# Kernel tuning notes

Measured on AMD Instinct MI355X. Metric: run time of the kernel, lower is better.

Reference implementation:

```python
import jax, jax.numpy as jnp
import numpy as np

NUM_HEADS = 4
LN_EPS = 1e-5


def _gcn_layer(src, dst, feats, skip_w, skip_b, msg_w, msg_b):
    # DGL GCNLayer: symmetric degree norm (from src rows), copy_u+sum aggregation,
    # msg linear + affine skip. No activation is applied in the original forward.
    n = feats.shape[0]
    deg = jax.ops.segment_sum(jnp.ones(src.shape, feats.dtype), src, num_segments=n)
    dinv = jnp.where(deg > 0, deg ** -0.5, jnp.zeros_like(deg))
    h = feats * dinv[:, None]                                  # [N, D]
    agg = jax.ops.segment_sum(h[src], dst, num_segments=n)     # scatter-sum over edges
    rst = agg * dinv[:, None]
    return rst @ msg_w.T + msg_b + feats @ skip_w.T + skip_b


def _layernorm(x, g, b):
    mu = jnp.mean(x, axis=-1, keepdims=True)
    var = jnp.mean((x - mu) ** 2, axis=-1, keepdims=True)
    return (x - mu) * jax.lax.rsqrt(var + LN_EPS) * g + b


def _cross_attention(x, seq, in_proj_w, in_proj_b, out_proj_w, out_proj_b, ln_g, ln_b):
    # Unbatched torch nn.MultiheadAttention(query=x [N,D], key=value=seq [S,D]).
    n, d = x.shape
    hd = d // NUM_HEADS
    wq, wk, wv = in_proj_w[:d], in_proj_w[d:2 * d], in_proj_w[2 * d:]
    bq, bk, bv = in_proj_b[:d], in_proj_b[d:2 * d], in_proj_b[2 * d:]
    q = (x @ wq.T + bq).reshape(n, NUM_HEADS, hd)
    k = (seq @ wk.T + bk).reshape(-1, NUM_HEADS, hd)
    v = (seq @ wv.T + bv).reshape(-1, NUM_HEADS, hd)
    scores = jnp.einsum('nhd,shd->hns', q, k) / jnp.sqrt(jnp.asarray(hd, x.dtype))
    attn = jax.nn.softmax(scores, axis=-1)
    o = jnp.einsum('hns,shd->nhd', attn, v).reshape(n, d)
    o = o @ out_proj_w.T + out_proj_b
    # dropout is identity in eval mode; residual + layernorm (num_cross_att == 1 path)
    return _layernorm(o + x, ln_g, ln_b)


def reference(x, seq_embeddings, src, dst, edge_label_index,
              skip_w0, skip_b0, msg_w0, msg_b0,
              skip_w1, skip_b1, msg_w1, msg_b1,
              in_proj_w, in_proj_b, out_proj_w, out_proj_b, ln_g, ln_b,
              weight1, weight2):
    x = _gcn_layer(src, dst, x, skip_w0, skip_b0, msg_w0, msg_b0)
    x = _gcn_layer(src, dst, x, skip_w1, skip_b1, msg_w1, msg_b1)
    x = _cross_attention(x, seq_embeddings, in_proj_w, in_proj_b,
                         out_proj_w, out_proj_b, ln_g, ln_b)
    # F.normalize: row-wise L2
    x = x / jnp.maximum(jnp.linalg.norm(x, axis=-1, keepdims=True), 1e-12)
    node_embedding = x
    p = jax.nn.relu(x @ weight1.T)                # dropout identity (eval)
    p = jax.nn.sigmoid(p @ weight2.T)[:, 0]       # [N]
    # dot edge decoding over last dim of size 1 -> elementwise product
    pred = p[edge_label_index[0]] * p[edge_label_index[1]]
    return pred, node_embedding


def setup_inputs() -> dict:
    key = jax.random.key(0)
    ks = jax.random.split(key, 20)
    N, E, S, D, K = 8192, 524288, 2048, 128, 100000
    s = 1.0 / np.sqrt(D)  # xavier-ish scale for weight matrices
    inp = {
        'x': jax.random.normal(ks[0], (N, D), jnp.float32),
        'seq_embeddings': jax.random.normal(ks[1], (S, D), jnp.float32),
        'src': jax.random.randint(ks[2], (E,), 0, N, jnp.int32),
        'dst': jax.random.randint(ks[3], (E,), 0, N, jnp.int32),
        'edge_label_index': jax.random.randint(ks[4], (2, K), 0, N, jnp.int32),
        'skip_w0': jax.random.normal(ks[5], (D, D), jnp.float32) * s,
        'skip_b0': jnp.zeros((D,), jnp.float32),
        'msg_w0': jax.random.normal(ks[6], (D, D), jnp.float32) * s,
        'msg_b0': jnp.zeros((D,), jnp.float32),
        'skip_w1': jax.random.normal(ks[7], (D, D), jnp.float32) * s,
        'skip_b1': jnp.zeros((D,), jnp.float32),
        'msg_w1': jax.random.normal(ks[8], (D, D), jnp.float32) * s,
        'msg_b1': jnp.zeros((D,), jnp.float32),
        'in_proj_w': jax.random.normal(ks[9], (3 * D, D), jnp.float32) * s,
        'in_proj_b': jnp.zeros((3 * D,), jnp.float32),
        'out_proj_w': jax.random.normal(ks[10], (D, D), jnp.float32) * s,
        'out_proj_b': jnp.zeros((D,), jnp.float32),
        'ln_g': jnp.ones((D,), jnp.float32),
        'ln_b': jnp.zeros((D,), jnp.float32),
        'weight1': jax.random.normal(ks[11], (D, D), jnp.float32) * s,
        'weight2': jax.random.normal(ks[12], (1, D), jnp.float32) * s,
    }
    return inp
```

## Files before the change

kernel.cpp:

```cpp
#include <hip/hip_runtime.h>
#include <math.h>

#define D 128
#define HB 128
#define FA_PS 88
#define SPLITS 4

typedef short bf16x4 __attribute__((ext_vector_type(4)));
typedef short bf16x8 __attribute__((ext_vector_type(8)));
typedef float f32x4 __attribute__((ext_vector_type(4)));

__device__ __forceinline__ float4 ld4(const float* p) { return *(const float4*)p; }

__device__ __forceinline__ short f2bf_r(float f) {
  return (short)((__float_as_uint(f) + 0x8000u) >> 16);
}
__device__ __forceinline__ float bf2f(short s) {
  return __uint_as_float(((unsigned)(unsigned short)s) << 16);
}
__device__ __forceinline__ unsigned pack_bf2(float a, float b) {
  unsigned ua = __float_as_uint(a) + 0x8000u;
  unsigned ub = __float_as_uint(b) + 0x8000u;
  return __builtin_amdgcn_perm(ub, ua, 0x07060302);
}

struct WSrc { const float* p[9]; };
__global__ __launch_bounds__(256) void prep_hist_kernel(
    WSrc ws, short* __restrict__ Wbf,
    const float* __restrict__ x, short* __restrict__ xbf, int* __restrict__ MkhI,
    const int* __restrict__ src, const int* __restrict__ dst,
    int* __restrict__ histd, int* __restrict__ hists, int E, int NB_COPY) {
  __shared__ int hd[8192];
  __shared__ int hs[8192];
  int b = blockIdx.x, t = threadIdx.x;
  if (b < NB_COPY) {
    if (b == 0 && t < 4) MkhI[t] = 0;
    if (b < 144) {
      int m = b >> 4, blk = b & 15;
      int i = (blk * 256 + t) * 4;
      float4 v = ld4(ws.p[m] + i);
      bf16x4 o = {f2bf_r(v.x), f2bf_r(v.y), f2bf_r(v.z), f2bf_r(v.w)};
      *(bf16x4*)&Wbf[m * 16384 + i] = o;
    } else {
      int i = ((b - 144) * 256 + t) * 4;
      float4 v = ld4(x + i);
      bf16x4 o = {f2bf_r(v.x), f2bf_r(v.y), f2bf_r(v.z), f2bf_r(v.w)};
      *(bf16x4*)&xbf[i] = o;
    }
    return;
  }
  int hb = b - NB_COPY;
  for (int i = t; i < 8192; i += 256) { hd[i] = 0; hs[i] = 0; }
  __syncthreads();
  int per = E / HB;
  int b0 = hb * per;
  for (int j = 0; j < per; j += 256) {
    int i = b0 + j + t;
    atomicAdd(&hd[dst[i]], 1);
    atomicAdd(&hs[src[i]], 1);
  }
  __syncthreads();
  for (int i = t; i < 8192; i += 256) {
    histd[hb * 8192 + i] = hd[i];
    hists[hb * 8192 + i] = hs[i];
  }
}

__global__ __launch_bounds__(256) void colsum_kernel(
    const int* __restrict__ histd, const int* __restrict__ hists,
    int* __restrict__ deg, float* __restrict__ dinv) {
  int v = blockIdx.x * 256 + threadIdx.x;
  int sd = 0, ss = 0;
  for (int b = 0; b < HB; ++b) { sd += histd[b * 8192 + v]; ss += hists[b * 8192 + v]; }
  deg[v] = sd;
  dinv[v] = ss > 0 ? rsqrtf((float)ss) : 0.f;
}

__global__ __launch_bounds__(1024) void scan8k_kernel(
    const int* __restrict__ deg, int* __restrict__ row_ptr, int N) {
  __shared__ int wtot[16];
  int t = threadIdx.x;
  int lane = t & 63, wv = t >> 6;
  int v0 = t * 8;
  int x[8]; int s = 0;
#pragma unroll
  for (int j = 0; j < 8; ++j) { x[j] = s; s += deg[v0 + j]; }
  int incl = s;
  for (int off = 1; off < 64; off <<= 1) {
    int y = __shfl_up(incl, off);
    if (lane >= off) incl += y;
  }
  if (lane == 63) wtot[wv] = incl;
  __syncthreads();
  if (t == 0) { int run = 0; for (int i = 0; i < 16; ++i) { int v = wtot[i]; wtot[i] = run; run += v; } }
  __syncthreads();
  int base = wtot[wv] + (incl - s);
#pragma unroll
  for (int j = 0; j < 8; ++j) row_ptr[v0 + j] = base + x[j];
  if (t == 1023) row_ptr[N] = base + s;
}

__global__ __launch_bounds__(256) void basegen_kernel(
    const int* __restrict__ histd, const int* __restrict__ row_ptr,
    int* __restrict__ base_arr) {
  int v = blockIdx.x * 256 + threadIdx.x;
  int run = row_ptr[v];
  for (int b = 0; b < HB; ++b) { base_arr[b * 8192 + v] = run; run += histd[b * 8192 + v]; }
}

__global__ __launch_bounds__(256) void scatter2_kernel(
    const int* __restrict__ src, const int* __restrict__ dst,
    const int* __restrict__ base_arr, int* __restrict__ csr_src, int E) {
  __shared__ int lh[8192];
  int t = threadIdx.x;
  for (int i = t; i < 8192; i += 256) lh[i] = 0;
  __syncthreads();
  int per = E / HB;
  int b0 = blockIdx.x * per;
  const int* __restrict__ bb = &base_arr[blockIdx.x * 8192];
  for (int j = 0; j < per; j += 256) {
    int i = b0 + j + t;
    int v = dst[i];
    int r = atomicAdd(&lh[v], 1);
    csr_src[bb[v] + r] = src[i];
  }
}

__global__ __launch_bounds__(128) void agg_kernel(
    const short* __restrict__ fbf, const float* __restrict__ dinv,
    const int* __restrict__ row_ptr, const int* __restrict__ csr_src,
    short* __restrict__ outbf) {
  __shared__ int idx[128];
  __shared__ float dv[128];
  __shared__ float red[8][128];
  int n = blockIdx.x, t = threadIdx.x;
  int grp = t >> 4, l16 = t & 15;
  int beg = row_ptr[n], end = row_ptr[n + 1];
  float a0[8] = {}, a1[8] = {}, a2[8] = {}, a3[8] = {};
  for (int c = beg; c < end; c += 128) {
    int j = c + t;
    if (j < end) { int s = csr_src[j]; idx[t] = s; dv[t] = dinv[s]; }
    __syncthreads();
    int cnt = min(128, end - c);
    int e = grp;
    for (; e + 24 < cnt; e += 32) {
      bf16x8 w0 = *(const bf16x8*)&fbf[(size_t)idx[e] * D + l16 * 8];
      bf16x8 w1 = *(const bf16x8*)&fbf[(size_t)idx[e + 8] * D + l16 * 8];
      bf16x8 w2 = *(const bf16x8*)&fbf[(size_t)idx[e + 16] * D + l16 * 8];
      bf16x8 w3 = *(const bf16x8*)&fbf[(size_t)idx[e + 24] * D + l16 * 8];
      float wt0 = dv[e], wt1 = dv[e + 8], wt2 = dv[e + 16], wt3 = dv[e + 24];
#pragma unroll
      for (int k = 0; k < 8; ++k) {
        a0[k] += bf2f(w0[k]) * wt0;
        a1[k] += bf2f(w1[k]) * wt1;
        a2[k] += bf2f(w2[k]) * wt2;
        a3[k] += bf2f(w3[k]) * wt3;
      }
    }
    for (; e < cnt; e += 8) {
      bf16x8 w0 = *(const bf16x8*)&fbf[(size_t)idx[e] * D + l16 * 8];
      float wt0 = dv[e];
#pragma unroll
      for (int k = 0; k < 8; ++k) a0[k] += bf2f(w0[k]) * wt0;
    }
    __syncthreads();
  }
#pragma unroll
  for (int k = 0; k < 8; ++k) a0[k] += a1[k] + a2[k] + a3[k];
  *(float4*)&red[grp][l16 * 8] = *(float4*)&a0[0];
  *(float4*)&red[grp][l16 * 8 + 4] = *(float4*)&a0[4];
  __syncthreads();
  if (t < 32) {
    int d0 = t * 4;
    float o[4] = {};
#pragma unroll
    for (int g = 0; g < 8; ++g) {
      o[0] += red[g][d0]; o[1] += red[g][d0 + 1];
      o[2] += red[g][d0 + 2]; o[3] += red[g][d0 + 3];
    }
    float w = dinv[n];
    bf16x4 ov = {f2bf_r(o[0] * w), f2bf_r(o[1] * w), f2bf_r(o[2] * w), f2bf_r(o[3] * w)};
    *(bf16x4*)&outbf[(size_t)n * D + d0] = ov;
  }
}

__device__ __forceinline__ void mfma_accum(const short* As, const short* __restrict__ W,
                                           int rt, int ch, int quad, int r16, f32x4* acc) {
#pragma unroll
  for (int ks = 0; ks < 4; ++ks) {
    bf16x8 af = *(bf16x8*)&As[(rt * 16 + r16) * 136 + ks * 32 + quad * 8];
#pragma unroll
    for (int nt = 0; nt < 4; ++nt) {
      bf16x8 bw = *(const bf16x8*)&W[(size_t)(ch * 64 + nt * 16 + r16) * D + ks * 32 + quad * 8];
      acc[nt] = __builtin_amdgcn_mfma_f32_16x16x32_bf16(af, bw, acc[nt], 0, 0, 0);
    }
  }
}

__device__ __forceinline__ void stage_A_f32(const float* __restrict__ A, int m0, short* As) {
  int row = threadIdx.x >> 3, seg = threadIdx.x & 7;
  const float* ap = &A[(size_t)(m0 + row) * D + seg * 16];
  float4 v0 = ld4(ap), v1 = ld4(ap + 4), v2 = ld4(ap + 8), v3 = ld4(ap + 12);
  bf16x8 w0 = {f2bf_r(v0.x), f2bf_r(v0.y), f2bf_r(v0.z), f2bf_r(v0.w),
               f2bf_r(v1.x), f2bf_r(v1.y), f2bf_r(v1.z), f2bf_r(v1.w)};
  bf16x8 w1 = {f2bf_r(v2.x), f2bf_r(v2.y), f2bf_r(v2.z), f2bf_r(v2.w),
               f2bf_r(v3.x), f2bf_r(v3.y), f2bf_r(v3.z), f2bf_r(v3.w)};
  *(bf16x8*)&As[row * 136 + seg * 16] = w0;
  *(bf16x8*)&As[row * 136 + seg * 16 + 8] = w1;
}

__device__ __forceinline__ void stage_A_bf16(const short* __restrict__ A, int m0, short* As) {
  int row = threadIdx.x >> 3, seg = threadIdx.x & 7;
  const short* ap = &A[(size_t)(m0 + row) * D + seg * 16];
  bf16x8 a0 = *(const bf16x8*)ap;
  bf16x8 a1 = *(const bf16x8*)(ap + 8);
  *(bf16x8*)&As[row * 136 + seg * 16] = a0;
  *(bf16x8*)&As[row * 136 + seg * 16 + 8] = a1;
}

__global__ __launch_bounds__(256) void gemm_gcn_kernel(
    const short* __restrict__ A1, const short* __restrict__ W1, const float* __restrict__ b1,
    const short* __restrict__ A2, const short* __restrict__ W2, const float* __restrict__ b2,
    short* __restrict__ Cbf, float* __restrict__ Cf) {
  __shared__ short As[32 * 136];
  const int t = threadIdx.x;
  const int m0 = blockIdx.x * 32;
  const int w = t >> 6, lane = t & 63, quad = lane >> 4, r16 = lane & 15;
  const int rt = w & 1, ch = w >> 1;
  f32x4 acc[4];
  f32x4 zz = {0.f, 0.f, 0.f, 0.f};
  acc[0] = zz; acc[1] = zz; acc[2] = zz; acc[3] = zz;
  stage_A_bf16(A1, m0, As);
  __syncthreads();
  mfma_accum(As, W1, rt, ch, quad, r16, acc);
  __syncthreads();
  stage_A_bf16(A2, m0, As);
  __syncthreads();
  mfma_accum(As, W2, rt, ch, quad, r16, acc);
#pragma unroll
  for (int nt = 0; nt < 4; ++nt) {
    int col = ch * 64 + nt * 16 + r16;
    float bias = b1[col] + b2[col];
#pragma unroll
    for (int g = 0; g < 4; ++g) {
      int row = m0 + rt * 16 + quad * 4 + g;
      float v = acc[nt][g] + bias;
      if (Cbf) Cbf[(size_t)row * D + col] = f2bf_r(v);
      if (Cf) Cf[(size_t)row * D + col] = v;
    }
  }
}

__global__ __launch_bounds__(256) void qkv_kernel(
    const float* __restrict__ B2, const float* __restrict__ seq,
    const short* __restrict__ Wq, const short* __restrict__ Wk, const short* __restrict__ Wv,
    const float* __restrict__ ipb,
    short* __restrict__ Qh, float* __restrict__ qn,
    short* __restrict__ Kh, int* __restrict__ MkhI,
    short* __restrict__ Vt, int N, int S) {
  __shared__ short As[32 * 136];
  __shared__ int lmax[4];
  const int t = threadIdx.x;
  const int b = blockIdx.x;
  const int w = t >> 6, lane = t & 63, quad = lane >> 4, r16 = lane & 15;
  const int rt = w & 1, ch = w >> 1;
  if (t < 4) lmax[t] = 0;
  f32x4 acc[4];
  f32x4 zz = {0.f, 0.f, 0.f, 0.f};
  acc[0] = zz; acc[1] = zz; acc[2] = zz; acc[3] = zz;
  const float SC = 0.25503473f;

  if (b < 256) {
    int m0 = b * 32;
    stage_A_f32(B2, m0, As);
    __syncthreads();
    mfma_accum(As, Wq, rt, ch, quad, r16, acc);
    float pq[4][2] = {};
#pragma unroll
    for (int nt = 0; nt < 4; ++nt) {
      int col = ch * 64 + nt * 16 + r16;
      int hq = col >> 5, dq = col & 31;
      float bias = ipb[col];
      int p = nt >> 1;
#pragma unroll
      for (int g = 0; g < 4; ++g) {
        int row = m0 + rt * 16 + quad * 4 + g;
        float vs = (acc[nt][g] + bias) * SC;
        Qh[((size_t)hq * N + row) * 32 + dq] = f2bf_r(vs);
        pq[g][p] += vs * vs;
      }
    }
#pragma unroll
    for (int mask = 1; mask < 16; mask <<= 1)
#pragma unroll
      for (int g = 0; g < 4; ++g) {
        pq[g][0] += __shfl_xor(pq[g][0], mask);
        pq[g][1] += __shfl_xor(pq[g][1], mask);
      }
    if (r16 == 0) {
#pragma unroll
      for (int g = 0; g < 4; ++g) {
        int row = m0 + rt * 16 + quad * 4 + g;
        qn[(ch * 2 + 0) * N + row] = sqrtf(pq[g][0]);
        qn[(ch * 2 + 1) * N + row] = sqrtf(pq[g][1]);
      }
    }
  } else if (b < 320) {
    int m0 = (b - 256) * 32;
    stage_A_f32(seq, m0, As);
    __syncthreads();
    mfma_accum(As, Wk, rt, ch, quad, r16, acc);
    float pk[4][2] = {};
#pragma unroll
    for (int nt = 0; nt < 4; ++nt) {
      int col = ch * 64 + nt * 16 + r16;
      int hk = col >> 5, dk = col & 31;
      float bias = ipb[128 + col];
      int p = nt >> 1;
#pragma unroll
      for (int g = 0; g < 4; ++g) {
        int key = m0 + rt * 16 + quad * 4 + g;
        float v = acc[nt][g] + bias;
        Kh[((size_t)hk * S + key) * 32 + dk] = f2bf_r(v);
        pk[g][p] += v * v;
      }
    }
#pragma unroll
    for (int mask = 1; mask < 16; mask <<= 1)
#pragma unroll
      for (int g = 0; g < 4; ++g) {
        pk[g][0] += __shfl_xor(pk[g][0], mask);
        pk[g][1] += __shfl_xor(pk[g][1], mask);
      }
    if (r16 == 0) {
#pragma unroll
      for (int g = 0; g < 4; ++g) {
        atomicMax(&lmax[ch * 2 + 0], __float_as_int(pk[g][0]));
        atomicMax(&lmax[ch * 2 + 1], __float_as_int(pk[g][1]));
      }
    }
    __syncthreads();
    if (t < 4) atomicMax(&MkhI[t], lmax[t]);
  } else {
    int m0 = (b - 320) * 32;
    stage_A_f32(seq, m0, As);
    __syncthreads();
    mfma_accum(As, Wv, rt, ch, quad, r16, acc);
#pragma unroll
    for (int nt = 0; nt < 4; ++nt) {
      int dim = ch * 64 + nt * 16 + r16;
      float bias = ipb[256 + dim];
#pragma unroll
      for (int g = 0; g < 4; ++g) {
        int s = m0 + rt * 16 + quad * 4 + g;
        int local = s & 63;
        int kp = (local & 15) * 4 + (local >> 4);
        int gcol = (s & ~63) + kp;
        Vt[(size_t)dim * S + gcol] = f2bf_r(acc[nt][g] + bias);
      }
    }
  }
}

__global__ __launch_bounds__(128, 8) void flash_kernel(
    const short* __restrict__ Qh, const short* __restrict__ Kh, const short* __restrict__ Vt,
    const float* __restrict__ qn, const int* __restrict__ MkhI,
    float* __restrict__ Osp, float* __restrict__ lbuf, int N, int S) {
  __shared__ short Ps[2][32 * FA_PS];
  const int wv = threadIdx.x >> 6;
  const int lane = threadIdx.x & 63;
  const int quad = lane >> 4, r16 = lane & 15;
  const int n0 = (blockIdx.x * 2 + wv) * 32;
  const int h = blockIdx.y;
  const int sp = blockIdx.z;
  float* O = Osp + (size_t)sp * N * D;
  const short* Kb = Kh + (size_t)h * S * 32;
  const short* Qb = Qh + (size_t)h * N * 32;
  short* Pw = Ps[wv];

  bf16x8 aq[2];
  aq[0] = *(const bf16x8*)&Qb[(size_t)(n0 + r16) * 32 + quad * 8];
  aq[1] = *(const bf16x8*)&Qb[(size_t)(n0 + 16 + r16) * 32 + quad * 8];

  float sqm = sqrtf(fmaxf(__int_as_float(MkhI[h]), 0.f));
  float msh[2][4];
#pragma unroll
  for (int rt = 0; rt < 2; ++rt)
#pragma unroll
    for (int g = 0; g < 4; ++g)
      msh[rt][g] = fminf(qn[h * N + n0 + rt * 16 + quad * 4 + g] * sqm, 57.7f);

  f32x4 o[2][2], lac[2];
  f32x4 zz = {0.f, 0.f, 0.f, 0.f};
  o[0][0] = zz; o[0][1] = zz; o[1][0] = zz; o[1][1] = zz;
  lac[0] = zz; lac[1] = zz;
  bf16x8 ones = {(short)0x3F80, (short)0x3F80, (short)0x3F80, (short)0x3F80,
                 (short)0x3F80, (short)0x3F80, (short)0x3F80, (short)0x3F80};

  const int span = S / SPLITS;
  const int c0 = sp * span;
  for (int c = c0; c < c0 + span; c += 64) {
    f32x4 s[2][4];
#pragma unroll
    for (int kt = 0; kt < 4; ++kt) {
      bf16x8 bk = *(const bf16x8*)&Kb[(size_t)(c + kt * 16 + r16) * 32 + quad * 8];
      f32x4 z = {0.f, 0.f, 0.f, 0.f};
      s[0][kt] = __builtin_amdgcn_mfma_f32_16x16x32_bf16(aq[0], bk, z, 0, 0, 0);
      s[1][kt] = __builtin_amdgcn_mfma_f32_16x16x32_bf16(aq[1], bk, z, 0, 0, 0);
    }
#pragma unroll
    for (int rt = 0; rt < 2; ++rt)
#pragma unroll
      for (int g = 0; g < 4; ++g) {
        float m = msh[rt][g];
        float p0 = exp2f(s[rt][0][g] - m);
        float p1 = exp2f(s[rt][1][g] - m);
        float p2 = exp2f(s[rt][2][g] - m);
        float p3 = exp2f(s[rt][3][g] - m);
        uint2 uv = {pack_bf2(p0, p1), pack_bf2(p2, p3)};
        *(uint2*)&Pw[(rt * 16 + quad * 4 + g) * FA_PS + r16 * 4] = uv;
      }
    bf16x8 bv[2][2];
#pragma unroll
    for (int kc = 0; kc < 2; ++kc)
#pragma unroll
      for (int nt = 0; nt < 2; ++nt)
        bv[kc][nt] = *(const bf16x8*)&Vt[(size_t)(h * 32 + nt * 16 + r16) * S + c + kc * 32 + quad * 8];
#pragma unroll
    for (int rt = 0; rt < 2; ++rt)
#pragma unroll
      for (int kc = 0; kc < 2; ++kc) {
        bf16x8 ap = *(bf16x8*)&Pw[(rt * 16 + r16) * FA_PS + kc * 32 + quad * 8];
        lac[rt] = __builtin_amdgcn_mfma_f32_16x16x32_bf16(ap, ones, lac[rt], 0, 0, 0);
#pragma unroll
        for (int nt = 0; nt < 2; ++nt)
          o[rt][nt] = __builtin_amdgcn_mfma_f32_16x16x32_bf16(ap, bv[kc][nt], o[rt][nt], 0, 0, 0);
      }
  }
#pragma unroll
  for (int rt = 0; rt < 2; ++rt)
#pragma unroll
    for (int g = 0; g < 4; ++g) {
      int row = n0 + rt * 16 + quad * 4 + g;
#pragma unroll
      for (int nt = 0; nt < 2; ++nt)
        O[(size_t)row * D + h * 32 + nt * 16 + r16] = o[rt][nt][g];
      if (r16 == 0) lbuf[(sp * 4 + h) * N + row] = lac[rt][g];
    }
}

__global__ __launch_bounds__(256) void gemm_op_kernel(
    const float* __restrict__ Osp, const float* __restrict__ lbuf,
    const short* __restrict__ W, const float* __restrict__ bias,
    const float* __restrict__ Rres, const float* __restrict__ ln_g,
    const float* __restrict__ ln_b, float* __restrict__ emb, int N) {
  __shared__ short As[32 * 136];
  __shared__ float Cs[32 * 132];
  const int t = threadIdx.x;
  const int m0 = blockIdx.x * 32;
  const int w = t >> 6, lane = t & 63, quad = lane >> 4, r16 = lane & 15;
  const int rt = w & 1, ch = w >> 1;
  {
    int row = t >> 3, seg = t & 7;
    int grow = m0 + row;
    int hh = seg >> 1;
    float l = 0.f;
#pragma unroll
    for (int s = 0; s < SPLITS; ++s) l += lbuf[(s * 4 + hh) * N + grow];
    float inv = 1.f / l;
    const float* p = &Osp[(size_t)grow * D + seg * 16];
    size_t st = (size_t)N * D;
    float a16[16] = {};
#pragma unroll
    for (int s = 0; s < SPLITS; ++s) {
#pragma unroll
      for (int q = 0; q < 4; ++q) {
        float4 a = ld4(p + s * st + q * 4);
        a16[q * 4 + 0] += a.x; a16[q * 4 + 1] += a.y;
        a16[q * 4 + 2] += a.z; a16[q * 4 + 3] += a.w;
      }
    }
#pragma unroll
    for (int k = 0; k < 16; ++k) a16[k] *= inv;
    bf16x8 w0 = {f2bf_r(a16[0]), f2bf_r(a16[1]), f2bf_r(a16[2]), f2bf_r(a16[3]),
                 f2bf_r(a16[4]), f2bf_r(a16[5]), f2bf_r(a16[6]), f2bf_r(a16[7])};
    bf16x8 w1 = {f2bf_r(a16[8]), f2bf_r(a16[9]), f2bf_r(a16[10]), f2bf_r(a16[11]),
                 f2bf_r(a16[12]), f2bf_r(a16[13]), f2bf_r(a16[14]), f2bf_r(a16[15])};
    *(bf16x8*)&As[row * 136 + seg * 16] = w0;
    *(bf16x8*)&As[row * 136 + seg * 16 + 8] = w1;
  }
  __syncthreads();
  f32x4 acc[4];
  f32x4 zz = {0.f, 0.f, 0.f, 0.f};
  acc[0] = zz; acc[1] = zz; acc[2] = zz; acc[3] = zz;
  mfma_accum(As, W, rt, ch, quad, r16, acc);
#pragma unroll
  for (int nt = 0; nt < 4; ++nt) {
    int col = ch * 64 + nt * 16 + r16;
    float bs = bias[col];
#pragma unroll
    for (int g = 0; g < 4; ++g) {
      int lr = rt * 16 + quad * 4 + g;
      Cs[lr * 132 + col] = acc[nt][g] + bs + Rres[(size_t)(m0 + lr) * D + col];
    }
  }
  __syncthreads();
  {
    int row = t >> 3, seg = t & 7;
    float xv[16];
#pragma unroll
    for (int q = 0; q < 4; ++q) {
      f32x4 v = *(f32x4*)&Cs[row * 132 + seg * 16 + q * 4];
      xv[q * 4] = v[0]; xv[q * 4 + 1] = v[1]; xv[q * 4 + 2] = v[2]; xv[q * 4 + 3] = v[3];
    }
    float s = 0.f, sq = 0.f;
#pragma unroll
    for (int k = 0; k < 16; ++k) { s += xv[k]; sq += xv[k] * xv[k]; }
#pragma unroll
    for (int mask = 1; mask < 8; mask <<= 1) { s += __shfl_xor(s, mask); sq += __shfl_xor(sq, mask); }
    float mu = s * (1.f / 128.f);
    float var = fmaxf(sq * (1.f / 128.f) - mu * mu, 0.f);
    float rs = rsqrtf(var + 1e-5f);
    float yv[16], nn = 0.f;
#pragma unroll
    for (int q = 0; q < 4; ++q) {
      float4 gg = ld4(&ln_g[seg * 16 + q * 4]);
      float4 bb = ld4(&ln_b[seg * 16 + q * 4]);
      float y0 = (xv[q * 4] - mu) * rs * gg.x + bb.x;
      float y1 = (xv[q * 4 + 1] - mu) * rs * gg.y + bb.y;
      float y2 = (xv[q * 4 + 2] - mu) * rs * gg.z + bb.z;
      float y3 = (xv[q * 4 + 3] - mu) * rs * gg.w + bb.w;
      yv[q * 4] = y0; yv[q * 4 + 1] = y1; yv[q * 4 + 2] = y2; yv[q * 4 + 3] = y3;
      nn += y0 * y0 + y1 * y1 + y2 * y2 + y3 * y3;
    }
#pragma unroll
    for (int mask = 1; mask < 8; mask <<= 1) nn += __shfl_xor(nn, mask);
    float inv = 1.f / fmaxf(sqrtf(nn), 1e-12f);
#pragma unroll
    for (int q = 0; q < 4; ++q) {
      float4 ov = {yv[q * 4] * inv, yv[q * 4 + 1] * inv, yv[q * 4 + 2] * inv, yv[q * 4 + 3] * inv};
      *(float4*)&emb[(size_t)(m0 + row) * D + seg * 16 + q * 4] = ov;
    }
  }
}

__global__ __launch_bounds__(256) void gemm_mlp_kernel(
    const float* __restrict__ emb, const short* __restrict__ W,
    const float* __restrict__ w2, float* __restrict__ pbuf) {
  __shared__ short As[32 * 136];
  __shared__ float part[32][2];
  const int t = threadIdx.x;
  const int m0 = blockIdx.x * 32;
  const int w = t >> 6, lane = t & 63, quad = lane >> 4, r16 = lane & 15;
  const int rt = w & 1, ch = w >> 1;
  stage_A_f32(emb, m0, As);
  __syncthreads();
  f32x4 acc[4];
  f32x4 zz = {0.f, 0.f, 0.f, 0.f};
  acc[0] = zz; acc[1] = zz; acc[2] = zz; acc[3] = zz;
  mfma_accum(As, W, rt, ch, quad, r16, acc);
  float pg[4] = {};
#pragma unroll
  for (int nt = 0; nt < 4; ++nt) {
    float wv = w2[ch * 64 + nt * 16 + r16];
#pragma unroll
    for (int g = 0; g < 4; ++g) pg[g] += fmaxf(acc[nt][g], 0.f) * wv;
  }
#pragma unroll
  for (int mask = 1; mask < 16; mask <<= 1)
#pragma unroll
    for (int g = 0; g < 4; ++g) pg[g] += __shfl_xor(pg[g], mask);
  if (r16 == 0) {
#pragma unroll
    for (int g = 0; g < 4; ++g) part[rt * 16 + quad * 4 + g][ch] = pg[g];
  }
  __syncthreads();
  if (t < 32) {
    float sv = part[t][0] + part[t][1];
    pbuf[m0 + t] = 1.f / (1.f + __expf(-sv));
  }
}

__global__ void pred_kernel(const float* __restrict__ p, const int* __restrict__ eli,
                            float* __restrict__ out, int K) {
  int i = blockIdx.x * blockDim.x + threadIdx.x;
  if (i < K) out[i] = p[eli[i]] * p[eli[K + i]];
}

extern "C" void kernel_launch(void* const* d_in, const int* in_sizes, int n_in,
                              void* d_out, int out_size, void* d_ws, size_t ws_size,
                              hipStream_t stream) {
  const float* x       = (const float*)d_in[0];
  const float* seq     = (const float*)d_in[1];
  const int* src       = (const int*)d_in[2];
  const int* dst       = (const int*)d_in[3];
  const int* eli       = (const int*)d_in[4];
  const float* skip_w0 = (const float*)d_in[5];
  const float* skip_b0 = (const float*)d_in[6];
  const float* msg_w0  = (const float*)d_in[7];
  const float* msg_b0  = (const float*)d_in[8];
  const float* skip_w1 = (const float*)d_in[9];
  const float* skip_b1 = (const float*)d_in[10];
  const float* msg_w1  = (const float*)d_in[11];
  const float* msg_b1  = (const float*)d_in[12];
  const float* ipw     = (const float*)d_in[13];
  const float* ipb     = (const float*)d_in[14];
  const float* opw     = (const float*)d_in[15];
  const float* opb     = (const float*)d_in[16];
  const float* ln_g    = (const float*)d_in[17];
  const float* ln_b    = (const float*)d_in[18];
  const float* w1      = (const float*)d_in[19];
  const float* w2      = (const float*)d_in[20];

  const int N  = in_sizes[0] / D;
  const int S  = in_sizes[1] / D;
  const int E  = in_sizes[2];
  const int Kp = in_sizes[4] / 2;

  float* ws    = (float*)d_ws;
  float* B2    = ws;
  float* Osp   = B2 + (size_t)N * D;
  short* xbf   = (short*)(Osp + (size_t)SPLITS * N * D);
  short* Abf   = xbf + (size_t)N * D;
  short* B1bf  = Abf + (size_t)N * D;
  short* Qh    = B1bf + (size_t)N * D;
  short* Kh    = Qh + (size_t)N * D;
  short* Vt    = Kh + (size_t)S * D;
  short* Wbf   = Vt + (size_t)D * S;
  float* qn    = (float*)(Wbf + 9 * 16384);
  float* lbuf  = qn + 4 * (size_t)N;
  float* dinv  = lbuf + 4 * (size_t)SPLITS * N;
  float* pbuf  = dinv + N;
  int*   MkhI  = (int*)(pbuf + N);
  int*   deg   = MkhI + 4;
  int* row_ptr = deg + N;
  int* csr_src = row_ptr + (N + 1);
  int* histd   = csr_src + E;
  int* hists   = histd + HB * 8192;
  int* base_arr= hists + HB * 8192;

  float* pred_out = (float*)d_out;
  float* emb_out  = pred_out + Kp;

  const short* w_skip0 = Wbf + 0 * 16384;
  const short* w_msg0  = Wbf + 1 * 16384;
  const short* w_skip1 = Wbf + 2 * 16384;
  const short* w_msg1  = Wbf + 3 * 16384;
  const short* w_q     = Wbf + 4 * 16384;
  const short* w_k     = Wbf + 5 * 16384;
  const short* w_v     = Wbf + 6 * 16384;
  const short* w_op    = Wbf + 7 * 16384;
  const short* w_m1    = Wbf + 8 * 16384;

  WSrc wsrc;
  wsrc.p[0] = skip_w0; wsrc.p[1] = msg_w0; wsrc.p[2] = skip_w1; wsrc.p[3] = msg_w1;
  wsrc.p[4] = ipw; wsrc.p[5] = ipw + D * D; wsrc.p[6] = ipw + 2 * D * D;
  wsrc.p[7] = opw; wsrc.p[8] = w1;

  const int NB_COPY = 144 + (N * D / 1024);
  prep_hist_kernel<<<NB_COPY + HB, 256, 0, stream>>>(
      wsrc, (short*)Wbf, x, xbf, MkhI, src, dst, histd, hists, E, NB_COPY);

  colsum_kernel<<<N / 256, 256, 0, stream>>>(histd, hists, deg, dinv);
  scan8k_kernel<<<1, 1024, 0, stream>>>(deg, row_ptr, N);
  basegen_kernel<<<N / 256, 256, 0, stream>>>(histd, row_ptr, base_arr);
  scatter2_kernel<<<HB, 256, 0, stream>>>(src, dst, base_arr, csr_src, E);

  agg_kernel<<<N, 128, 0, stream>>>(xbf, dinv, row_ptr, csr_src, Abf);
  gemm_gcn_kernel<<<N / 32, 256, 0, stream>>>(Abf, w_msg0, msg_b0, xbf, w_skip0, skip_b0, B1bf, nullptr);
  agg_kernel<<<N, 128, 0, stream>>>(B1bf, dinv, row_ptr, csr_src, Abf);
  gemm_gcn_kernel<<<N / 32, 256, 0, stream>>>(Abf, w_msg1, msg_b1, B1bf, w_skip1, skip_b1, nullptr, B2);

  qkv_kernel<<<N / 32 + 2 * (S / 32), 256, 0, stream>>>(
      B2, seq, w_q, w_k, w_v, ipb, Qh, qn, Kh, MkhI, Vt, N, S);

  dim3 fgrid(N / 64, 4, SPLITS);
  flash_kernel<<<fgrid, 128, 0, stream>>>(Qh, Kh, Vt, qn, MkhI, Osp, lbuf, N, S);
  gemm_op_kernel<<<N / 32, 256, 0, stream>>>(Osp, lbuf, w_op, opb, B2, ln_g, ln_b, emb_out, N);

  gemm_mlp_kernel<<<N / 32, 256, 0, stream>>>(emb_out, w_m1, w2, pbuf);
  pred_kernel<<<(Kp + 255) / 256, 256, 0, stream>>>(pbuf, eli, pred_out, Kp);
}
```

Baseline: 238.7 us.

## Fuse Q projection into GCN GEMM, fuse MLP into out-proj, shrink histograms

```diff
diff --git a/kernel.cpp b/kernel.cpp
--- a/kernel.cpp
+++ b/kernel.cpp
@@ -29,7 +29,8 @@
     WSrc ws, short* __restrict__ Wbf,
     const float* __restrict__ x, short* __restrict__ xbf, int* __restrict__ MkhI,
     const int* __restrict__ src, const int* __restrict__ dst,
-    int* __restrict__ histd, int* __restrict__ hists, int E, int NB_COPY) {
+    unsigned short* __restrict__ histd, unsigned short* __restrict__ hists,
+    int E, int NB_COPY) {
   __shared__ int hd[8192];
   __shared__ int hs[8192];
   int b = blockIdx.x, t = threadIdx.x;
@@ -61,13 +62,13 @@
   }
   __syncthreads();
   for (int i = t; i < 8192; i += 256) {
-    histd[hb * 8192 + i] = hd[i];
-    hists[hb * 8192 + i] = hs[i];
+    histd[hb * 8192 + i] = (unsigned short)hd[i];
+    hists[hb * 8192 + i] = (unsigned short)hs[i];
   }
 }
 
 __global__ __launch_bounds__(256) void colsum_kernel(
-    const int* __restrict__ histd, const int* __restrict__ hists,
+    const unsigned short* __restrict__ histd, const unsigned short* __restrict__ hists,
     int* __restrict__ deg, float* __restrict__ dinv) {
   int v = blockIdx.x * 256 + threadIdx.x;
   int sd = 0, ss = 0;
@@ -101,7 +102,7 @@
 }
 
 __global__ __launch_bounds__(256) void basegen_kernel(
-    const int* __restrict__ histd, const int* __restrict__ row_ptr,
+    const unsigned short* __restrict__ histd, const int* __restrict__ row_ptr,
     int* __restrict__ base_arr) {
   int v = blockIdx.x * 256 + threadIdx.x;
   int run = row_ptr[v];
@@ -221,7 +222,7 @@
 __global__ __launch_bounds__(256) void gemm_gcn_kernel(
     const short* __restrict__ A1, const short* __restrict__ W1, const float* __restrict__ b1,
     const short* __restrict__ A2, const short* __restrict__ W2, const float* __restrict__ b2,
-    short* __restrict__ Cbf, float* __restrict__ Cf) {
+    short* __restrict__ Cbf) {
   __shared__ short As[32 * 136];
   const int t = threadIdx.x;
   const int m0 = blockIdx.x * 32;
@@ -244,20 +245,87 @@
 #pragma unroll
     for (int g = 0; g < 4; ++g) {
       int row = m0 + rt * 16 + quad * 4 + g;
+      Cbf[(size_t)row * D + col] = f2bf_r(acc[nt][g] + bias);
+    }
+  }
+}
+
+__global__ __launch_bounds__(256) void gemm_gcn2q_kernel(
+    const short* __restrict__ A1, const short* __restrict__ Wmsg, const float* __restrict__ bmsg,
+    const short* __restrict__ B1bf, const short* __restrict__ Wskip, const float* __restrict__ bskip,
+    const short* __restrict__ Wq, const float* __restrict__ ipb,
+    float* __restrict__ B2, short* __restrict__ Qh, float* __restrict__ qn, int N) {
+  __shared__ short As[32 * 136];
+  const int t = threadIdx.x;
+  const int m0 = blockIdx.x * 32;
+  const int w = t >> 6, lane = t & 63, quad = lane >> 4, r16 = lane & 15;
+  const int rt = w & 1, ch = w >> 1;
+  f32x4 acc[4];
+  f32x4 zz = {0.f, 0.f, 0.f, 0.f};
+  acc[0] = zz; acc[1] = zz; acc[2] = zz; acc[3] = zz;
+  stage_A_bf16(A1, m0, As);
+  __syncthreads();
+  mfma_accum(As, Wmsg, rt, ch, quad, r16, acc);
+  __syncthreads();
+  stage_A_bf16(B1bf, m0, As);
+  __syncthreads();
+  mfma_accum(As, Wskip, rt, ch, quad, r16, acc);
+  __syncthreads();
+#pragma unroll
+  for (int nt = 0; nt < 4; ++nt) {
+    int col = ch * 64 + nt * 16 + r16;
+    float bias = bmsg[col] + bskip[col];
+#pragma unroll
+    for (int g = 0; g < 4; ++g) {
+      int lr = rt * 16 + quad * 4 + g;
       float v = acc[nt][g] + bias;
-      if (Cbf) Cbf[(size_t)row * D + col] = f2bf_r(v);
-      if (Cf) Cf[(size_t)row * D + col] = v;
-    }
-  }
-}
-
-__global__ __launch_bounds__(256) void qkv_kernel(
-    const float* __restrict__ B2, const float* __restrict__ seq,
-    const short* __restrict__ Wq, const short* __restrict__ Wk, const short* __restrict__ Wv,
+      B2[(size_t)(m0 + lr) * D + col] = v;
+      As[lr * 136 + col] = f2bf_r(v);
+    }
+  }
+  __syncthreads();
+  f32x4 qa[4];
+  qa[0] = zz; qa[1] = zz; qa[2] = zz; qa[3] = zz;
+  mfma_accum(As, Wq, rt, ch, quad, r16, qa);
+  const float SC = 0.25503473f;
+  float pq[4][2] = {};
+#pragma unroll
+  for (int nt = 0; nt < 4; ++nt) {
+    int col = ch * 64 + nt * 16 + r16;
+    int hq = col >> 5, dq = col & 31;
+    float bias = ipb[col];
+    int p = nt >> 1;
+#pragma unroll
+    for (int g = 0; g < 4; ++g) {
+      int row = m0 + rt * 16 + quad * 4 + g;
+      float vs = (qa[nt][g] + bias) * SC;
+      Qh[((size_t)hq * N + row) * 32 + dq] = f2bf_r(vs);
+      pq[g][p] += vs * vs;
+    }
+  }
+#pragma unroll
+  for (int mask = 1; mask < 16; mask <<= 1)
+#pragma unroll
+    for (int g = 0; g < 4; ++g) {
+      pq[g][0] += __shfl_xor(pq[g][0], mask);
+      pq[g][1] += __shfl_xor(pq[g][1], mask);
+    }
+  if (r16 == 0) {
+#pragma unroll
+    for (int g = 0; g < 4; ++g) {
+      int row = m0 + rt * 16 + quad * 4 + g;
+      qn[(ch * 2 + 0) * N + row] = sqrtf(pq[g][0]);
+      qn[(ch * 2 + 1) * N + row] = sqrtf(pq[g][1]);
+    }
+  }
+}
+
+__global__ __launch_bounds__(256) void kv_kernel(
+    const float* __restrict__ seq,
+    const short* __restrict__ Wk, const short* __restrict__ Wv,
     const float* __restrict__ ipb,
-    short* __restrict__ Qh, float* __restrict__ qn,
     short* __restrict__ Kh, int* __restrict__ MkhI,
-    short* __restrict__ Vt, int N, int S) {
+    short* __restrict__ Vt, int S) {
   __shared__ short As[32 * 136];
   __shared__ int lmax[4];
   const int t = threadIdx.x;
@@ -268,45 +336,9 @@
   f32x4 acc[4];
   f32x4 zz = {0.f, 0.f, 0.f, 0.f};
   acc[0] = zz; acc[1] = zz; acc[2] = zz; acc[3] = zz;
-  const float SC = 0.25503473f;
-
-  if (b < 256) {
+
+  if (b < 64) {
     int m0 = b * 32;
-    stage_A_f32(B2, m0, As);
-    __syncthreads();
-    mfma_accum(As, Wq, rt, ch, quad, r16, acc);
-    float pq[4][2] = {};
-#pragma unroll
-    for (int nt = 0; nt < 4; ++nt) {
-      int col = ch * 64 + nt * 16 + r16;
-      int hq = col >> 5, dq = col & 31;
-      float bias = ipb[col];
-      int p = nt >> 1;
-#pragma unroll
-      for (int g = 0; g < 4; ++g) {
-        int row = m0 + rt * 16 + quad * 4 + g;
-        float vs = (acc[nt][g] + bias) * SC;
-        Qh[((size_t)hq * N + row) * 32 + dq] = f2bf_r(vs);
-        pq[g][p] += vs * vs;
-      }
-    }
-#pragma unroll
-    for (int mask = 1; mask < 16; mask <<= 1)
-#pragma unroll
-      for (int g = 0; g < 4; ++g) {
-        pq[g][0] += __shfl_xor(pq[g][0], mask);
-        pq[g][1] += __shfl_xor(pq[g][1], mask);
-      }
-    if (r16 == 0) {
-#pragma unroll
-      for (int g = 0; g < 4; ++g) {
-        int row = m0 + rt * 16 + quad * 4 + g;
-        qn[(ch * 2 + 0) * N + row] = sqrtf(pq[g][0]);
-        qn[(ch * 2 + 1) * N + row] = sqrtf(pq[g][1]);
-      }
-    }
-  } else if (b < 320) {
-    int m0 = (b - 256) * 32;
     stage_A_f32(seq, m0, As);
     __syncthreads();
     mfma_accum(As, Wk, rt, ch, quad, r16, acc);
@@ -342,7 +374,7 @@
     __syncthreads();
     if (t < 4) atomicMax(&MkhI[t], lmax[t]);
   } else {
-    int m0 = (b - 320) * 32;
+    int m0 = (b - 64) * 32;
     stage_A_f32(seq, m0, As);
     __syncthreads();
     mfma_accum(As, Wv, rt, ch, quad, r16, acc);
@@ -449,13 +481,16 @@
     }
 }
 
-__global__ __launch_bounds__(256) void gemm_op_kernel(
+__global__ __launch_bounds__(256) void gemm_op_mlp_kernel(
     const float* __restrict__ Osp, const float* __restrict__ lbuf,
     const short* __restrict__ W, const float* __restrict__ bias,
     const float* __restrict__ Rres, const float* __restrict__ ln_g,
-    const float* __restrict__ ln_b, float* __restrict__ emb, int N) {
+    const float* __restrict__ ln_b, float* __restrict__ emb,
+    const short* __restrict__ Wm1, const float* __restrict__ w2,
+    float* __restrict__ pbuf, int N) {
   __shared__ short As[32 * 136];
   __shared__ float Cs[32 * 132];
+  __shared__ float part[32][2];
   const int t = threadIdx.x;
   const int m0 = blockIdx.x * 32;
   const int w = t >> 6, lane = t & 63, quad = lane >> 4, r16 = lane & 15;
@@ -536,35 +571,31 @@
 #pragma unroll
     for (int mask = 1; mask < 8; mask <<= 1) nn += __shfl_xor(nn, mask);
     float inv = 1.f / fmaxf(sqrtf(nn), 1e-12f);
+    float ev[16];
+#pragma unroll
+    for (int k = 0; k < 16; ++k) ev[k] = yv[k] * inv;
 #pragma unroll
     for (int q = 0; q < 4; ++q) {
-      float4 ov = {yv[q * 4] * inv, yv[q * 4 + 1] * inv, yv[q * 4 + 2] * inv, yv[q * 4 + 3] * inv};
+      float4 ov = {ev[q * 4], ev[q * 4 + 1], ev[q * 4 + 2], ev[q * 4 + 3]};
       *(float4*)&emb[(size_t)(m0 + row) * D + seg * 16 + q * 4] = ov;
     }
-  }
-}
-
-__global__ __launch_bounds__(256) void gemm_mlp_kernel(
-    const float* __restrict__ emb, const short* __restrict__ W,
-    const float* __restrict__ w2, float* __restrict__ pbuf) {
-  __shared__ short As[32 * 136];
-  __shared__ float part[32][2];
-  const int t = threadIdx.x;
-  const int m0 = blockIdx.x * 32;
-  const int w = t >> 6, lane = t & 63, quad = lane >> 4, r16 = lane & 15;
-  const int rt = w & 1, ch = w >> 1;
-  stage_A_f32(emb, m0, As);
-  __syncthreads();
-  f32x4 acc[4];
-  f32x4 zz = {0.f, 0.f, 0.f, 0.f};
-  acc[0] = zz; acc[1] = zz; acc[2] = zz; acc[3] = zz;
-  mfma_accum(As, W, rt, ch, quad, r16, acc);
+    bf16x8 e0 = {f2bf_r(ev[0]), f2bf_r(ev[1]), f2bf_r(ev[2]), f2bf_r(ev[3]),
+                 f2bf_r(ev[4]), f2bf_r(ev[5]), f2bf_r(ev[6]), f2bf_r(ev[7])};
+    bf16x8 e1 = {f2bf_r(ev[8]), f2bf_r(ev[9]), f2bf_r(ev[10]), f2bf_r(ev[11]),
+                 f2bf_r(ev[12]), f2bf_r(ev[13]), f2bf_r(ev[14]), f2bf_r(ev[15])};
+    *(bf16x8*)&As[row * 136 + seg * 16] = e0;
+    *(bf16x8*)&As[row * 136 + seg * 16 + 8] = e1;
+  }
+  __syncthreads();
+  f32x4 ma[4];
+  ma[0] = zz; ma[1] = zz; ma[2] = zz; ma[3] = zz;
+  mfma_accum(As, Wm1, rt, ch, quad, r16, ma);
   float pg[4] = {};
 #pragma unroll
   for (int nt = 0; nt < 4; ++nt) {
-    float wv = w2[ch * 64 + nt * 16 + r16];
-#pragma unroll
-    for (int g = 0; g < 4; ++g) pg[g] += fmaxf(acc[nt][g], 0.f) * wv;
+    float wv2 = w2[ch * 64 + nt * 16 + r16];
+#pragma unroll
+    for (int g = 0; g < 4; ++g) pg[g] += fmaxf(ma[nt][g], 0.f) * wv2;
   }
 #pragma unroll
   for (int mask = 1; mask < 16; mask <<= 1)
@@ -635,9 +666,9 @@
   int*   deg   = MkhI + 4;
   int* row_ptr = deg + N;
   int* csr_src = row_ptr + (N + 1);
-  int* histd   = csr_src + E;
-  int* hists   = histd + HB * 8192;
-  int* base_arr= hists + HB * 8192;
+  int* base_arr= csr_src + E;
+  unsigned short* histd = (unsigned short*)(base_arr + HB * 8192);
+  unsigned short* hists = histd + HB * 8192;
 
   float* pred_out = (float*)d_out;
   float* emb_out  = pred_out + Kp;
@@ -667,17 +698,17 @@
   scatter2_kernel<<<HB, 256, 0, stream>>>(src, dst, base_arr, csr_src, E);
 
   agg_kernel<<<N, 128, 0, stream>>>(xbf, dinv, row_ptr, csr_src, Abf);
-  gemm_gcn_kernel<<<N / 32, 256, 0, stream>>>(Abf, w_msg0, msg_b0, xbf, w_skip0, skip_b0, B1bf, nullptr);
+  gemm_gcn_kernel<<<N / 32, 256, 0, stream>>>(Abf, w_msg0, msg_b0, xbf, w_skip0, skip_b0, B1bf);
   agg_kernel<<<N, 128, 0, stream>>>(B1bf, dinv, row_ptr, csr_src, Abf);
-  gemm_gcn_kernel<<<N / 32, 256, 0, stream>>>(Abf, w_msg1, msg_b1, B1bf, w_skip1, skip_b1, nullptr, B2);
-
-  qkv_kernel<<<N / 32 + 2 * (S / 32), 256, 0, stream>>>(
-      B2, seq, w_q, w_k, w_v, ipb, Qh, qn, Kh, MkhI, Vt, N, S);
+  gemm_gcn2q_kernel<<<N / 32, 256, 0, stream>>>(Abf, w_msg1, msg_b1, B1bf, w_skip1, skip_b1,
+                                                w_q, ipb, B2, Qh, qn, N);
+
+  kv_kernel<<<128, 256, 0, stream>>>(seq, w_k, w_v, ipb, Kh, MkhI, Vt, S);
 
   dim3 fgrid(N / 64, 4, SPLITS);
   flash_kernel<<<fgrid, 128, 0, stream>>>(Qh, Kh, Vt, qn, MkhI, Osp, lbuf, N, S);
-  gemm_op_kernel<<<N / 32, 256, 0, stream>>>(Osp, lbuf, w_op, opb, B2, ln_g, ln_b, emb_out, N);
-
-  gemm_mlp_kernel<<<N / 32, 256, 0, stream>>>(emb_out, w_m1, w2, pbuf);
+
+  gemm_op_mlp_kernel<<<N / 32, 256, 0, stream>>>(Osp, lbuf, w_op, opb, B2, ln_g, ln_b,
+                                                 emb_out, w_m1, w2, pbuf, N);
   pred_kernel<<<(Kp + 255) / 256, 256, 0, stream>>>(pbuf, eli, pred_out, Kp);
 }
```

Result: no change. 240.7 us (+0.8%).
